# Kernel tuning notes

Measured on AMD Instinct MI355X. Metric: run time of the kernel, lower is better.

## Reference

```python
import jax, jax.numpy as jnp
import numpy as np

D_MODEL = 256
N_HEADS = 4
D_FF = 1024
N = 6144
N_DOMS = 1024
LN_EPS = 1e-5
NEG_INF = -1e30


def setup_inputs() -> dict:
    key = jax.random.key(0)
    ks = jax.random.split(key, 10)
    x = jax.random.normal(ks[0], (N, D_MODEL), dtype=jnp.float32)
    pulse_to_dom_idx = jnp.sort(jax.random.randint(ks[1], (N,), 0, N_DOMS, dtype=jnp.int32))
    s = 0.02
    return {
        "x": x,
        "pulse_to_dom_idx": pulse_to_dom_idx,
        "qkv_w": jax.random.normal(ks[2], (D_MODEL, 3 * D_MODEL), dtype=jnp.float32) * s,
        "qkv_b": jnp.zeros((3 * D_MODEL,), dtype=jnp.float32),
        "out_w": jax.random.normal(ks[3], (D_MODEL, D_MODEL), dtype=jnp.float32) * s,
        "out_b": jnp.zeros((D_MODEL,), dtype=jnp.float32),
        "ff_w1": jax.random.normal(ks[4], (D_MODEL, D_FF), dtype=jnp.float32) * s,
        "ff_b1": jnp.zeros((D_FF,), dtype=jnp.float32),
        "ff_w2": jax.random.normal(ks[5], (D_FF, D_MODEL), dtype=jnp.float32) * s,
        "ff_b2": jnp.zeros((D_MODEL,), dtype=jnp.float32),
        "ln1_g": jnp.ones((D_MODEL,), dtype=jnp.float32),
        "ln1_b": jnp.zeros((D_MODEL,), dtype=jnp.float32),
        "ln2_g": jnp.ones((D_MODEL,), dtype=jnp.float32),
        "ln2_b": jnp.zeros((D_MODEL,), dtype=jnp.float32),
    }


def _layer_norm(x, g, b):
    mu = jnp.mean(x, axis=-1, keepdims=True)
    var = jnp.mean(jnp.square(x - mu), axis=-1, keepdims=True)
    return (x - mu) * jax.lax.rsqrt(var + LN_EPS) * g + b


def reference(x, pulse_to_dom_idx, qkv_w, qkv_b, out_w, out_b,
              ff_w1, ff_b1, ff_w2, ff_b2, ln1_g, ln1_b, ln2_g, ln2_b):
    n, d = x.shape
    hd = d // N_HEADS
    # --- document-masked multi-head attention (dense, matching FlexAttention score_mod) ---
    qkv = x @ qkv_w + qkv_b                      # (N, 3D)
    q, k, v = jnp.split(qkv, 3, axis=-1)
    q = q.reshape(n, N_HEADS, hd)
    k = k.reshape(n, N_HEADS, hd)
    v = v.reshape(n, N_HEADS, hd)
    scores = jnp.einsum('qhd,khd->hqk', q, k) / jnp.sqrt(jnp.float32(hd))  # (H, N, N)
    same_doc = pulse_to_dom_idx[:, None] == pulse_to_dom_idx[None, :]      # (N, N)
    scores = jnp.where(same_doc[None], scores, NEG_INF)
    attn = jax.nn.softmax(scores, axis=-1)
    attn_out = jnp.einsum('hqk,khd->qhd', attn, v).reshape(n, d)
    attn_out = attn_out @ out_w + out_b
    # --- residual + norm + FFN + residual + norm (dropout in eval mode) ---
    x = _layer_norm(x + attn_out, ln1_g, ln1_b)
    ff = jax.nn.gelu(x @ ff_w1 + ff_b1, approximate=False) @ ff_w2 + ff_b2
    x = _layer_norm(x + ff, ln2_g, ln2_b)
    return x
```

## Files before the change

### kernel.cpp

```cpp
#include <hip/hip_runtime.h>
#include <hip/hip_bf16.h>
#include <math.h>

constexpr int NP  = 6144;
constexpr int DM  = 256;
constexpr int DFF = 1024;
constexpr float LNEPS = 1e-5f;

typedef __attribute__((ext_vector_type(8))) short short8;
typedef __attribute__((ext_vector_type(4))) short short4v;
typedef __attribute__((ext_vector_type(4))) float f32x4;

__device__ __forceinline__ short f2bf(float f) {
    unsigned u = __builtin_bit_cast(unsigned, f);
    unsigned r = u + 0x7FFFu + ((u >> 16) & 1u);
    return (short)(r >> 16);
}
__device__ __forceinline__ float bf2f(short s) {
    unsigned u = ((unsigned)(unsigned short)s) << 16;
    return __builtin_bit_cast(float, u);
}

#define GLOAD16(gp, lp)                                                        \
    __builtin_amdgcn_global_load_lds(                                          \
        (const __attribute__((address_space(1))) unsigned int*)(gp),           \
        (__attribute__((address_space(3))) unsigned int*)(lp), 16, 0, 0)

__device__ __forceinline__ int lds_idx(int row, int chunk) {
    return row * 64 + ((chunk ^ (row & 7)) * 8);
}
__device__ __forceinline__ int lds_idx128(int row, int chunk) {
    return row * 128 + ((chunk ^ (row & 7)) * 8);
}

__global__ __launch_bounds__(256) void prep_kernel(
    const float* __restrict__ qkv_w, const float* __restrict__ out_w,
    const float* __restrict__ ff_w1, const float* __restrict__ ff_w2,
    short* __restrict__ qkvT, short* __restrict__ outT,
    short* __restrict__ ff1T, short* __restrict__ ff2T,
    const int* __restrict__ dom, int* __restrict__ seg_s,
    int* __restrict__ seg_e, const float* __restrict__ x,
    short* __restrict__ xB) {
    int b = blockIdx.x;
    if (b >= 792) {
        int i = (b - 792) * 2048 + threadIdx.x * 8;
        float4 a0 = *(const float4*)&x[i];
        float4 a1 = *(const float4*)&x[i + 4];
        short8 v = { f2bf(a0.x), f2bf(a0.y), f2bf(a0.z), f2bf(a0.w),
                     f2bf(a1.x), f2bf(a1.y), f2bf(a1.z), f2bf(a1.w) };
        *(short8*)&xB[i] = v;
        return;
    }
    if (b >= 768) {
        int i = (b - 768) * 256 + threadIdx.x;
        if (i >= NP) return;
        int d = dom[i];
        int s = i;
        while (s > 0 && dom[s - 1] == d) --s;
        int e = i + 1;
        while (e < NP && dom[e] == d) ++e;
        seg_s[i] = s;
        seg_e[i] = e;
        return;
    }
    const float* src;
    short* dst;
    int K, Nn;
    if (b < 192)      { src = qkv_w; dst = qkvT; K = 256;  Nn = 768; }
    else if (b < 256) { b -= 192; src = out_w; dst = outT; K = 256;  Nn = 256; }
    else if (b < 512) { b -= 256; src = ff_w1; dst = ff1T; K = 256;  Nn = 1024; }
    else              { b -= 512; src = ff_w2; dst = ff2T; K = 1024; Nn = 256; }
    int tpr = Nn / 32;
    int k0 = (b / tpr) * 32, n0 = (b % tpr) * 32;

    __shared__ float lds[32][36];
    int t = threadIdx.x;
    {
        int k = t >> 3, n = (t & 7) * 4;
        *(float4*)&lds[k][n] = *(const float4*)&src[(size_t)(k0 + k) * Nn + n0 + n];
    }
    __syncthreads();
    {
        int n = t >> 3, ks = (t & 7) * 4;
        short4v o = { f2bf(lds[ks + 0][n]), f2bf(lds[ks + 1][n]),
                      f2bf(lds[ks + 2][n]), f2bf(lds[ks + 3][n]) };
        *(short4v*)&dst[(size_t)(n0 + n) * K + k0 + ks] = o;
    }
}

template <int EPI>
__global__ __launch_bounds__(256) void mgemm64(
    const short* __restrict__ A, const short* __restrict__ Bt,
    const float* __restrict__ bias, const short* __restrict__ res,
    void* __restrict__ Cv, int Nn, int K) {
    __shared__ __align__(16) short As[64 * 128];
    __shared__ __align__(16) short Bs[64 * 128];

    const int tid = threadIdx.x, lane = tid & 63, w = tid >> 6;
    const int wm = (w >> 1) * 32, wn = (w & 1) * 32;

    const int nx = gridDim.x;
    const int bid = blockIdx.y * nx + blockIdx.x;
    const int q = (nx * gridDim.y) >> 3;
    const int id2 = (bid & 7) * q + (bid >> 3);
    const int rowBase = (id2 / nx) * 64, colBase = (id2 % nx) * 64;

    const int lr4 = lane >> 4;
    const int c16 = lane & 15;
    const int fr = lane & 15, g4 = lane >> 4;

    f32x4 acc[2][2];
#pragma unroll
    for (int i = 0; i < 2; ++i)
#pragma unroll
        for (int j = 0; j < 2; ++j) acc[i][j] = f32x4{0.f, 0.f, 0.f, 0.f};

    for (int k0 = 0; k0 < K; k0 += 128) {
#pragma unroll
        for (int i = 0; i < 4; ++i) {
            int g = w * 4 + i;
            int row = g * 4 + lr4;
            int sc = c16 ^ (row & 7);
            GLOAD16(A  + (size_t)(rowBase + row) * K + k0 + sc * 8, &As[g * 512]);
            GLOAD16(Bt + (size_t)(colBase + row) * K + k0 + sc * 8, &Bs[g * 512]);
        }
        __syncthreads();

#pragma unroll
        for (int kk = 0; kk < 4; ++kk) {
            int j = kk * 4 + g4;
            short8 af[2], bfv[2];
#pragma unroll
            for (int f = 0; f < 2; ++f) {
                af[f]  = *(const short8*)&As[lds_idx128(wm + f * 16 + fr, j)];
                bfv[f] = *(const short8*)&Bs[lds_idx128(wn + f * 16 + fr, j)];
            }
#pragma unroll
            for (int fm = 0; fm < 2; ++fm)
#pragma unroll
                for (int fn = 0; fn < 2; ++fn)
                    acc[fm][fn] = __builtin_amdgcn_mfma_f32_16x16x32_bf16(
                        af[fm], bfv[fn], acc[fm][fn], 0, 0, 0);
        }
        __syncthreads();
    }

    const int cr = g4 * 4;
#pragma unroll
    for (int fm = 0; fm < 2; ++fm)
#pragma unroll
        for (int fn = 0; fn < 2; ++fn) {
            int c = colBase + wn + fn * 16 + fr;
            float bv = bias[c];
#pragma unroll
            for (int j = 0; j < 4; ++j) {
                int r = rowBase + wm + fm * 16 + cr + j;
                float v = acc[fm][fn][j] + bv;
                if (EPI == 1) v = 0.5f * v * (1.0f + erff(v * 0.70710678118654752f));
                if (EPI == 2)
                    ((float*)Cv)[(size_t)r * Nn + c] =
                        v + bf2f(res[(size_t)r * 256 + c]);
                else
                    ((short*)Cv)[(size_t)r * Nn + c] = f2bf(v);
            }
        }
}

__global__ __launch_bounds__(256) void ln_kernel(
    const float* __restrict__ in, const float* __restrict__ g,
    const float* __restrict__ b, float* __restrict__ out) {
    int wid = blockIdx.x * 4 + (threadIdx.x >> 6);
    int lane = threadIdx.x & 63;

    float4 v = ((const float4*)(in + (size_t)wid * 256))[lane];
    float s = v.x + v.y + v.z + v.w;
#pragma unroll
    for (int off = 32; off; off >>= 1) s += __shfl_xor(s, off);
    float mu = s * (1.0f / 256.0f);
    float dx = v.x - mu, dy = v.y - mu, dz = v.z - mu, dw = v.w - mu;
    float ss = dx * dx + dy * dy + dz * dz + dw * dw;
#pragma unroll
    for (int off = 32; off; off >>= 1) ss += __shfl_xor(ss, off);
    float rstd = rsqrtf(ss * (1.0f / 256.0f) + LNEPS);

    float4 gg = ((const float4*)g)[lane];
    float4 bb = ((const float4*)b)[lane];
    float4 o;
    o.x = dx * rstd * gg.x + bb.x;
    o.y = dy * rstd * gg.y + bb.y;
    o.z = dz * rstd * gg.z + bb.z;
    o.w = dw * rstd * gg.w + bb.w;
    ((float4*)(out + (size_t)wid * 256))[lane] = o;
}

__global__ __launch_bounds__(512) void attnln_kernel(
    const short* __restrict__ qkvB, const int* __restrict__ seg_s,
    const int* __restrict__ seg_e, const short* __restrict__ outT,
    const float* __restrict__ out_b, const float* __restrict__ xres,
    const float* __restrict__ gw, const float* __restrict__ bw,
    short* __restrict__ x1) {
    __shared__ __align__(16) short As[16 * 256];
    __shared__ __align__(16) short Bs[256 * 64];
    __shared__ float r1[8][16], r2[8][16];

    const int tid = threadIdx.x, lane = tid & 63, w = tid >> 6;
    const int rowBase = blockIdx.x * 16;
    const int lr = lane >> 3, sc = (lane & 7) ^ lr;
    const int fr = lane & 15, g4 = lane >> 4;

    {
        const int l8 = lane & 7;
        const int G  = (w << 3) | (lane >> 3);
        int r = G >> 2, h = G & 3;
        int row = rowBase + r;
        short8 qv = *(const short8*)&qkvB[(size_t)row * 768 + h * 64 + l8 * 8];
        float qd[8];
#pragma unroll
        for (int e = 0; e < 8; ++e) qd[e] = bf2f(qv[e]);
        int ss = seg_s[row], ee = seg_e[row];
        float m = -INFINITY, l = 0.0f;
        float acc[8] = {0.f, 0.f, 0.f, 0.f, 0.f, 0.f, 0.f, 0.f};
        for (int j = ss; j < ee; ++j) {
            short8 kv = *(const short8*)&qkvB[(size_t)j * 768 + 256 + h * 64 + l8 * 8];
            short8 vv = *(const short8*)&qkvB[(size_t)j * 768 + 512 + h * 64 + l8 * 8];
            float prod = 0.f;
#pragma unroll
            for (int e = 0; e < 8; ++e) prod += qd[e] * bf2f(kv[e]);
            prod += __shfl_xor(prod, 1);
            prod += __shfl_xor(prod, 2);
            prod += __shfl_xor(prod, 4);
            float score = prod * 0.125f;
            float mn = fmaxf(m, score);
            float scale = __expf(m - mn);
            float p = __expf(score - mn);
            l = l * scale + p;
#pragma unroll
            for (int e = 0; e < 8; ++e) acc[e] = acc[e] * scale + p * bf2f(vv[e]);
            m = mn;
        }
        float inv = 1.0f / l;
        int c = h * 8 + l8;
        short8 o;
#pragma unroll
        for (int e = 0; e < 8; ++e) o[e] = f2bf(acc[e] * inv);
        *(short8*)&As[r * 256 + ((c ^ (r & 7)) * 8)] = o;
    }
    __syncthreads();

    f32x4 acc[2];
    acc[0] = f32x4{0.f, 0.f, 0.f, 0.f};
    acc[1] = f32x4{0.f, 0.f, 0.f, 0.f};

    for (int k0 = 0; k0 < 256; k0 += 64) {
#pragma unroll
        for (int i = 0; i < 4; ++i) {
            int g = w * 4 + i;
            GLOAD16(outT + (size_t)(g * 8 + lr) * 256 + k0 + sc * 8, &Bs[g * 512]);
        }
        __syncthreads();
#pragma unroll
        for (int kk = 0; kk < 2; ++kk) {
            int j = kk * 4 + g4;
            int cj = (k0 >> 3) + j;
            short8 af = *(const short8*)&As[fr * 256 + ((cj ^ (fr & 7)) * 8)];
            short8 bfv[2];
#pragma unroll
            for (int fn = 0; fn < 2; ++fn)
                bfv[fn] = *(const short8*)&Bs[lds_idx(w * 32 + fn * 16 + fr, j)];
#pragma unroll
            for (int fn = 0; fn < 2; ++fn)
                acc[fn] = __builtin_amdgcn_mfma_f32_16x16x32_bf16(
                    af, bfv[fn], acc[fn], 0, 0, 0);
        }
        __syncthreads();
    }

    float v[2][4], p1[4], p2[4];
#pragma unroll
    for (int j = 0; j < 4; ++j) { p1[j] = 0.f; p2[j] = 0.f; }
#pragma unroll
    for (int fn = 0; fn < 2; ++fn) {
        int c = w * 32 + fn * 16 + fr;
        float bv = out_b[c];
#pragma unroll
        for (int j = 0; j < 4; ++j) {
            int r = rowBase + g4 * 4 + j;
            float t = acc[fn][j] + bv + xres[(size_t)r * 256 + c];
            v[fn][j] = t;
            p1[j] += t;
            p2[j] += t * t;
        }
    }
#pragma unroll
    for (int m = 1; m < 16; m <<= 1)
#pragma unroll
        for (int j = 0; j < 4; ++j) {
            p1[j] += __shfl_xor(p1[j], m);
            p2[j] += __shfl_xor(p2[j], m);
        }
    if (fr == 0) {
#pragma unroll
        for (int j = 0; j < 4; ++j) {
            r1[w][g4 * 4 + j] = p1[j];
            r2[w][g4 * 4 + j] = p2[j];
        }
    }
    __syncthreads();
#pragma unroll
    for (int j = 0; j < 4; ++j) {
        int rl = g4 * 4 + j;
        int r = rowBase + rl;
        float s1 = 0.f, s2 = 0.f;
#pragma unroll
        for (int ww = 0; ww < 8; ++ww) { s1 += r1[ww][rl]; s2 += r2[ww][rl]; }
        float mu = s1 * (1.0f / 256.0f);
        float var = s2 * (1.0f / 256.0f) - mu * mu;
        float rstd = rsqrtf(var + LNEPS);
#pragma unroll
        for (int fn = 0; fn < 2; ++fn) {
            int c = w * 32 + fn * 16 + fr;
            float o = (v[fn][j] - mu) * rstd * gw[c] + bw[c];
            x1[(size_t)r * 256 + c] = f2bf(o);
        }
    }
}

extern "C" void kernel_launch(void* const* d_in, const int* in_sizes, int n_in,
                              void* d_out, int out_size, void* d_ws, size_t ws_size,
                              hipStream_t stream) {
    const float* x      = (const float*)d_in[0];
    const int*   dom    = (const int*)d_in[1];
    const float* qkv_w  = (const float*)d_in[2];
    const float* qkv_b  = (const float*)d_in[3];
    const float* out_w  = (const float*)d_in[4];
    const float* out_b  = (const float*)d_in[5];
    const float* ff_w1  = (const float*)d_in[6];
    const float* ff_b1  = (const float*)d_in[7];
    const float* ff_w2  = (const float*)d_in[8];
    const float* ff_b2  = (const float*)d_in[9];
    const float* ln1_g  = (const float*)d_in[10];
    const float* ln1_b  = (const float*)d_in[11];
    const float* ln2_g  = (const float*)d_in[12];
    const float* ln2_b  = (const float*)d_in[13];
    float* out = (float*)d_out;

    short* xB     = (short*)d_ws;
    short* qkvB   = xB + (size_t)NP * 256;
    short* x1     = qkvB + (size_t)NP * 768;
    short* hB     = x1 + (size_t)NP * 256;
    short* qkvT   = hB + (size_t)NP * 1024;
    short* outT   = qkvT + 768 * 256;
    short* ff1T   = outT + 256 * 256;
    short* ff2T   = ff1T + 1024 * 256;
    int* seg_s    = (int*)(ff2T + 256 * 1024);
    int* seg_e    = seg_s + NP;
    float* y      = (float*)(seg_e + NP);

    prep_kernel<<<1560, 256, 0, stream>>>(qkv_w, out_w, ff_w1, ff_w2,
                                          qkvT, outT, ff1T, ff2T,
                                          dom, seg_s, seg_e, x, xB);

    mgemm64<0><<<dim3(768 / 64, NP / 64), 256, 0, stream>>>(
        xB, qkvT, qkv_b, nullptr, qkvB, 768, 256);

    attnln_kernel<<<NP / 16, 512, 0, stream>>>(
        qkvB, seg_s, seg_e, outT, out_b, x, ln1_g, ln1_b, x1);

    mgemm64<1><<<dim3(DFF / 64, NP / 64), 256, 0, stream>>>(
        x1, ff1T, ff_b1, nullptr, hB, 1024, 256);

    mgemm64<2><<<dim3(DM / 64, NP / 64), 256, 0, stream>>>(
        hB, ff2T, ff_b2, x1, y, 256, 1024);

    ln_kernel<<<NP / 4, 256, 0, stream>>>(y, ln2_g, ln2_b, out);
}
```

Before: 60.03 us.

## Use 128x64 GEMM tiles with K=128 stages for QKV and FF1 GEMMs

Adds a 128x64-tile MFMA GEMM kernel, where each wave computes a 64x32 sub-tile and the K loop steps by 128 with XOR-swizzled LDS staging. It replaces the 64x64 kernel for the QKV projection and the first FFN layer (with GELU). The attention kernel's out-projection also moves to K=128 stages, halving its barrier count. The goal is more operand reuse per LDS load and fewer syncs, at the cost of more LDS and registers per block and half as many blocks.

```diff
diff --git a/kernel.cpp b/kernel.cpp
--- a/kernel.cpp
+++ b/kernel.cpp
@@ -89,6 +89,86 @@
 }
 
 template <int EPI>
+__global__ __launch_bounds__(256) void mgemm128x64(
+    const short* __restrict__ A, const short* __restrict__ Bt,
+    const float* __restrict__ bias, short* __restrict__ C, int Nn, int K) {
+    __shared__ __align__(16) short As[128 * 128];
+    __shared__ __align__(16) short Bs[64 * 128];
+
+    const int tid = threadIdx.x, lane = tid & 63, w = tid >> 6;
+    const int wm = (w >> 1) * 64, wn = (w & 1) * 32;
+
+    const int nx = gridDim.x;
+    const int bid = blockIdx.y * nx + blockIdx.x;
+    const int q = (nx * gridDim.y) >> 3;
+    const int id2 = (bid & 7) * q + (bid >> 3);
+    const int rowBase = (id2 / nx) * 128, colBase = (id2 % nx) * 64;
+
+    const int lr4 = lane >> 4;
+    const int c16 = lane & 15;
+    const int fr = lane & 15, g4 = lane >> 4;
+
+    f32x4 acc[4][2];
+#pragma unroll
+    for (int i = 0; i < 4; ++i)
+#pragma unroll
+        for (int j = 0; j < 2; ++j) acc[i][j] = f32x4{0.f, 0.f, 0.f, 0.f};
+
+    for (int k0 = 0; k0 < K; k0 += 128) {
+#pragma unroll
+        for (int i = 0; i < 12; ++i) {
+            int g = w * 12 + i;
+            if (g < 32) {
+                int row = g * 4 + lr4;
+                int sc = c16 ^ (row & 7);
+                GLOAD16(A + (size_t)(rowBase + row) * K + k0 + sc * 8, &As[g * 512]);
+            } else {
+                int row = (g - 32) * 4 + lr4;
+                int sc = c16 ^ (row & 7);
+                GLOAD16(Bt + (size_t)(colBase + row) * K + k0 + sc * 8,
+                        &Bs[(g - 32) * 512]);
+            }
+        }
+        __syncthreads();
+
+#pragma unroll
+        for (int kk = 0; kk < 4; ++kk) {
+            int j = kk * 4 + g4;
+            short8 af[4], bfv[2];
+#pragma unroll
+            for (int f = 0; f < 4; ++f)
+                af[f] = *(const short8*)&As[lds_idx128(wm + f * 16 + fr, j)];
+#pragma unroll
+            for (int f = 0; f < 2; ++f)
+                bfv[f] = *(const short8*)&Bs[lds_idx128(wn + f * 16 + fr, j)];
+#pragma unroll
+            for (int fm = 0; fm < 4; ++fm)
+#pragma unroll
+                for (int fn = 0; fn < 2; ++fn)
+                    acc[fm][fn] = __builtin_amdgcn_mfma_f32_16x16x32_bf16(
+                        af[fm], bfv[fn], acc[fm][fn], 0, 0, 0);
+        }
+        __syncthreads();
+    }
+
+    const int cr = g4 * 4;
+#pragma unroll
+    for (int fm = 0; fm < 4; ++fm)
+#pragma unroll
+        for (int fn = 0; fn < 2; ++fn) {
+            int c = colBase + wn + fn * 16 + fr;
+            float bv = bias[c];
+#pragma unroll
+            for (int j = 0; j < 4; ++j) {
+                int r = rowBase + wm + fm * 16 + cr + j;
+                float v = acc[fm][fn][j] + bv;
+                if (EPI == 1) v = 0.5f * v * (1.0f + erff(v * 0.70710678118654752f));
+                C[(size_t)r * Nn + c] = f2bf(v);
+            }
+        }
+}
+
+template <int EPI>
 __global__ __launch_bounds__(256) void mgemm64(
     const short* __restrict__ A, const short* __restrict__ Bt,
     const float* __restrict__ bias, const short* __restrict__ res,
@@ -200,12 +280,12 @@
     const float* __restrict__ gw, const float* __restrict__ bw,
     short* __restrict__ x1) {
     __shared__ __align__(16) short As[16 * 256];
-    __shared__ __align__(16) short Bs[256 * 64];
+    __shared__ __align__(16) short Bs[256 * 128];
     __shared__ float r1[8][16], r2[8][16];
 
     const int tid = threadIdx.x, lane = tid & 63, w = tid >> 6;
     const int rowBase = blockIdx.x * 16;
-    const int lr = lane >> 3, sc = (lane & 7) ^ lr;
+    const int lr4 = lane >> 4, c16 = lane & 15;
     const int fr = lane & 15, g4 = lane >> 4;
 
     {
@@ -251,22 +331,24 @@
     acc[0] = f32x4{0.f, 0.f, 0.f, 0.f};
     acc[1] = f32x4{0.f, 0.f, 0.f, 0.f};
 
-    for (int k0 = 0; k0 < 256; k0 += 64) {
-#pragma unroll
-        for (int i = 0; i < 4; ++i) {
-            int g = w * 4 + i;
-            GLOAD16(outT + (size_t)(g * 8 + lr) * 256 + k0 + sc * 8, &Bs[g * 512]);
-        }
-        __syncthreads();
-#pragma unroll
-        for (int kk = 0; kk < 2; ++kk) {
+    for (int k0 = 0; k0 < 256; k0 += 128) {
+#pragma unroll
+        for (int i = 0; i < 8; ++i) {
+            int g = w * 8 + i;
+            int row = g * 4 + lr4;
+            int sc = c16 ^ (row & 7);
+            GLOAD16(outT + (size_t)row * 256 + k0 + sc * 8, &Bs[g * 512]);
+        }
+        __syncthreads();
+#pragma unroll
+        for (int kk = 0; kk < 4; ++kk) {
             int j = kk * 4 + g4;
             int cj = (k0 >> 3) + j;
             short8 af = *(const short8*)&As[fr * 256 + ((cj ^ (fr & 7)) * 8)];
             short8 bfv[2];
 #pragma unroll
             for (int fn = 0; fn < 2; ++fn)
-                bfv[fn] = *(const short8*)&Bs[lds_idx(w * 32 + fn * 16 + fr, j)];
+                bfv[fn] = *(const short8*)&Bs[lds_idx128(w * 32 + fn * 16 + fr, j)];
 #pragma unroll
             for (int fn = 0; fn < 2; ++fn)
                 acc[fn] = __builtin_amdgcn_mfma_f32_16x16x32_bf16(
@@ -360,14 +442,14 @@
                                           qkvT, outT, ff1T, ff2T,
                                           dom, seg_s, seg_e, x, xB);
 
-    mgemm64<0><<<dim3(768 / 64, NP / 64), 256, 0, stream>>>(
-        xB, qkvT, qkv_b, nullptr, qkvB, 768, 256);
+    mgemm128x64<0><<<dim3(768 / 64, NP / 128), 256, 0, stream>>>(
+        xB, qkvT, qkv_b, qkvB, 768, 256);
 
     attnln_kernel<<<NP / 16, 512, 0, stream>>>(
         qkvB, seg_s, seg_e, outT, out_b, x, ln1_g, ln1_b, x1);
 
-    mgemm64<1><<<dim3(DFF / 64, NP / 64), 256, 0, stream>>>(
-        x1, ff1T, ff_b1, nullptr, hB, 1024, 256);
+    mgemm128x64<1><<<dim3(DFF / 64, NP / 128), 256, 0, stream>>>(
+        x1, ff1T, ff_b1, hB, 1024, 256);
 
     mgemm64<2><<<dim3(DM / 64, NP / 64), 256, 0, stream>>>(
         hB, ff2T, ff_b2, x1, y, 256, 1024);
```

Result: no change. 59.67 us (-0.6%).
